# Performance work log

Measured on AMD Instinct MI355X. Metric: run time of the kernel, lower is better.

Reference implementation:

```python
import jax, jax.numpy as jnp
import numpy as np

B, IN_DIM, H1, H2, HID, SPEC_H, OUT, E = 16384, 1024, 2048, 2048, 1024, 2048, 1, 8


def setup_inputs() -> dict:
    key = jax.random.key(0)
    ks = jax.random.split(key, 12)

    def lin(k, fan_in, shape):
        # torch nn.Linear default init: U(-1/sqrt(fan_in), 1/sqrt(fan_in))
        bound = 1.0 / np.sqrt(fan_in)
        return jax.random.uniform(k, shape, jnp.float32, -bound, bound)

    return {
        "x": jax.random.normal(ks[0], (B, IN_DIM), jnp.float32),
        "d": jax.random.randint(ks[1], (B,), 0, E, jnp.int64),
        # shared encoder: Linear(IN,H1)+ReLU, Linear(H1,H2)+ReLU, Linear(H2,HID)
        "enc_W0": lin(ks[2], IN_DIM, (IN_DIM, H1)),
        "enc_b0": lin(ks[3], IN_DIM, (H1,)),
        "enc_W1": lin(ks[4], H1, (H1, H2)),
        "enc_b1": lin(ks[5], H1, (H2,)),
        "enc_W2": lin(ks[6], H2, (H2, HID)),
        "enc_b2": lin(ks[7], H2, (HID,)),
        # per-domain heads: Linear(HID,SPEC_H)+ReLU, Linear(SPEC_H,OUT)
        "spec_W1": lin(ks[8], HID, (E, HID, SPEC_H)),
        "spec_b1": lin(ks[9], HID, (E, SPEC_H)),
        "spec_W2": lin(ks[10], SPEC_H, (E, SPEC_H, OUT)),
        "spec_b2": lin(ks[11], SPEC_H, (E, OUT)),
    }


def reference(x, d, enc_W0, enc_b0, enc_W1, enc_b1, enc_W2, enc_b2,
              spec_W1, spec_b1, spec_W2, spec_b2):
    # Shared encoder (dropout is identity in eval mode)
    z = jax.nn.relu(x @ enc_W0 + enc_b0)        # [B, H1]
    z = jax.nn.relu(z @ enc_W1 + enc_b1)        # [B, H2]
    z = z @ enc_W2 + enc_b2                     # [B, HID]

    # Domain-routed heads: compute each expert on the full batch, combine by mask.
    n_experts = spec_W1.shape[0]
    out = jnp.zeros((z.shape[0], spec_W2.shape[-1]), dtype=z.dtype)  # [B, OUT]
    for e in range(n_experts):
        h = jax.nn.relu(z @ spec_W1[e] + spec_b1[e])  # [B, SPEC_H]
        y = h @ spec_W2[e] + spec_b2[e]               # [B, OUT]
        out = out + jnp.where((d == e)[:, None], y, jnp.zeros_like(y))
    return out
```

## Files before the change

### kernel.cpp

```cpp
#include <hip/hip_runtime.h>
#include <hip/hip_bf16.h>
#include <stdint.h>

#define B_SZ   16384
#define IN_DIM 1024
#define H1     2048
#define H2     2048
#define HID    1024
#define SPEC_H 2048
#define NE     8
#define ETILES 72

typedef __bf16 bf16x8 __attribute__((ext_vector_type(8)));
typedef float  f32x4  __attribute__((ext_vector_type(4)));
typedef ushort us8    __attribute__((ext_vector_type(8)));

__device__ __forceinline__ ushort f2bf(float f) {
  uint32_t u = __float_as_uint(f);
  u += 0x7FFF + ((u >> 16) & 1);
  return (ushort)(u >> 16);
}

__device__ __forceinline__ void gl_lds16(const void* g, void* l) {
  __builtin_amdgcn_global_load_lds(
      (const __attribute__((address_space(1))) void*)g,
      (__attribute__((address_space(3))) void*)l, 16, 0, 0);
}


struct TransDesc { const float* src; ushort* dst; int K, N, nx, base; };

struct PrepArgs {
  TransDesc td[4];
  const float* x; ushort* xb;
  const int* d; int* counts; const float* sb2; float* out;
  int castBase;
  int cntBase;
};

__global__ void prep_all(PrepArgs pa) {
  int g = blockIdx.x;
  int t = threadIdx.x;
  if (g >= pa.cntBase) {
    __shared__ int hist[NE];
    if (t < NE) hist[t] = 0;
    __syncthreads();
    int i = (g - pa.cntBase) * 256 + t;
    int e = pa.d[i];
    atomicAdd(&hist[e], 1);
    pa.out[i] = pa.sb2[e];
    __syncthreads();
    if (t < NE) atomicAdd(&pa.counts[t], hist[t]);
    return;
  }
  if (g >= pa.castBase) {
    size_t i = (size_t)(g - pa.castBase) * 4096 + (size_t)t * 16;
    float4 v0 = *(const float4*)(pa.x + i);
    float4 v1 = *(const float4*)(pa.x + i + 4);
    float4 v2 = *(const float4*)(pa.x + i + 8);
    float4 v3 = *(const float4*)(pa.x + i + 12);
    uint32_t p0 = f2bf(v0.x) | ((uint32_t)f2bf(v0.y) << 16);
    uint32_t p1 = f2bf(v0.z) | ((uint32_t)f2bf(v0.w) << 16);
    uint32_t p2 = f2bf(v1.x) | ((uint32_t)f2bf(v1.y) << 16);
    uint32_t p3 = f2bf(v1.z) | ((uint32_t)f2bf(v1.w) << 16);
    uint32_t p4 = f2bf(v2.x) | ((uint32_t)f2bf(v2.y) << 16);
    uint32_t p5 = f2bf(v2.z) | ((uint32_t)f2bf(v2.w) << 16);
    uint32_t p6 = f2bf(v3.x) | ((uint32_t)f2bf(v3.y) << 16);
    uint32_t p7 = f2bf(v3.z) | ((uint32_t)f2bf(v3.w) << 16);
    int4 pkA = {(int)p0, (int)p1, (int)p2, (int)p3};
    int4 pkB = {(int)p4, (int)p5, (int)p6, (int)p7};
    *(int4*)(pa.xb + i) = pkA;
    *(int4*)(pa.xb + i + 8) = pkB;
    return;
  }
  __shared__ float tile[64][65];
  int wsel = 0;
#pragma unroll
  for (int i = 1; i < 4; ++i)
    if (g >= pa.td[i].base) wsel = i;
  TransDesc dd = pa.td[wsel];
  int local = g - dd.base;
  int per = dd.nx * (dd.K >> 6);
  int z = local / per;
  int r = local - z * per;
  int bx = r % dd.nx, by = r / dd.nx;
  int n0 = bx * 64, k0 = by * 64;
  const float* src = dd.src + (size_t)z * dd.K * dd.N;
  ushort* dst = dd.dst + (size_t)z * dd.K * dd.N;
  int lk = t >> 4;
  int ln4 = (t & 15) * 4;
#pragma unroll
  for (int j = 0; j < 4; ++j) {
    int k = lk + j * 16;
    float4 v = *(const float4*)(src + (size_t)(k0 + k) * dd.N + n0 + ln4);
    tile[ln4 + 0][k] = v.x;
    tile[ln4 + 1][k] = v.y;
    tile[ln4 + 2][k] = v.z;
    tile[ln4 + 3][k] = v.w;
  }
  __syncthreads();
  int kc = (t & 7) * 8;
  int nb = t >> 3;
#pragma unroll
  for (int j = 0; j < 2; ++j) {
    int nn = nb + j * 32;
    us8 o;
#pragma unroll
    for (int q = 0; q < 8; ++q) o[q] = f2bf(tile[nn][kc + q]);
    *(us8*)(dst + (size_t)(n0 + nn) * dd.K + k0 + kc) = o;
  }
}


__global__ void build_k(const int* __restrict__ counts, int* __restrict__ catalog,
                        int* __restrict__ poff, int* __restrict__ cursors) {
  if (threadIdx.x == 0) {
    int off = 0;
    for (int e = 0; e < NE; ++e) {
      poff[e] = off * 256;
      int nt = (counts[e] + 255) >> 8;
      for (int i = 0; i < nt; ++i) catalog[off + i] = e;
      off += nt;
      cursors[e] = 0;
    }
    for (int i = off; i < ETILES; ++i) catalog[i] = -1;
  }
}

__global__ void scatter_k(const int* __restrict__ d, const int* __restrict__ poff,
                          int* __restrict__ cursors, int* __restrict__ perm) {
  __shared__ int wcnt[4][NE];
  __shared__ int basee[NE];
  int t = threadIdx.x;
  int i = blockIdx.x * 256 + t;
  int e = d[i];
  int w = t >> 6, lane = t & 63;
  uint64_t mymask = 0;
#pragma unroll
  for (int ee = 0; ee < NE; ++ee) {
    uint64_t mm = __ballot(e == ee);
    if (lane == 0) wcnt[w][ee] = __popcll(mm);
    if (e == ee) mymask = mm;
  }
  int rank = __popcll(mymask & ((1ull << lane) - 1ull));
  __syncthreads();
  if (t < NE) {
    int s = 0;
#pragma unroll
    for (int ww = 0; ww < 4; ++ww) { int c = wcnt[ww][t]; wcnt[ww][t] = s; s += c; }
    basee[t] = atomicAdd(&cursors[t], s);
  }
  __syncthreads();
  int pos = basee[e] + wcnt[w][e] + rank;
  perm[poff[e] + pos] = i;
}


template <int RELU>
__global__ __launch_bounds__(256, 2) void gemm_bias_256(
    const ushort* __restrict__ A, const ushort* __restrict__ Bt,
    const float* __restrict__ bias, ushort* __restrict__ C,
    int M, int N, int K, int lognx) {
  __shared__ __align__(16) ushort lA[256 * 64];
  __shared__ __align__(16) ushort lB[128 * 64];
  const int t = threadIdx.x;
  const int h = blockIdx.x;
  const int g = h >> 3;
  const int nx = 1 << lognx;
  const int by = (h & 7) + ((g >> lognx) << 3);
  const int bx = g & (nx - 1);
  const int m0 = by * 256, n0 = bx * 128;
  const int w = t >> 6, lane = t & 63;
  const int wm = (w >> 1) * 128, wn = (w & 1) * 64;
  const int q = lane >> 4, rl = lane & 15;

  f32x4 acc[8][4];
#pragma unroll
  for (int mi = 0; mi < 8; ++mi)
#pragma unroll
    for (int ni = 0; ni < 4; ++ni) acc[mi][ni] = 0.0f;

  const int row_s = t >> 3;
  const int pch_s = t & 7;

  for (int k0 = 0; k0 < K; k0 += 64) {
    __syncthreads();
#pragma unroll
    for (int j = 0; j < 8; ++j) {
      int row = j * 32 + row_s;
      int gch = pch_s ^ (row & 7);
      gl_lds16(A + (size_t)(m0 + row) * K + k0 + gch * 8, lA + j * 2048 + w * 512);
    }
#pragma unroll
    for (int j = 0; j < 4; ++j) {
      int row = j * 32 + row_s;
      int gch = pch_s ^ (row & 7);
      gl_lds16(Bt + (size_t)(n0 + row) * K + k0 + gch * 8, lB + j * 2048 + w * 512);
    }
    __syncthreads();
#pragma unroll
    for (int kk = 0; kk < 2; ++kk) {
      bf16x8 bfr[4];
#pragma unroll
      for (int i = 0; i < 4; ++i) {
        int pc = (kk * 4 + q) ^ (rl & 7);
        bfr[i] = __builtin_bit_cast(bf16x8, *(const int4*)(lB + (wn + i * 16 + rl) * 64 + pc * 8));
      }
#pragma unroll
      for (int mi = 0; mi < 8; ++mi) {
        int pc = (kk * 4 + q) ^ (rl & 7);
        bf16x8 af = __builtin_bit_cast(bf16x8, *(const int4*)(lA + (wm + mi * 16 + rl) * 64 + pc * 8));
#pragma unroll
        for (int ni = 0; ni < 4; ++ni)
          acc[mi][ni] = __builtin_amdgcn_mfma_f32_16x16x32_bf16(af, bfr[ni], acc[mi][ni], 0, 0, 0);
      }
    }
  }

  float bv[4];
#pragma unroll
  for (int ni = 0; ni < 4; ++ni) bv[ni] = bias[n0 + wn + ni * 16 + rl];
#pragma unroll
  for (int mi = 0; mi < 8; ++mi) {
    int rg = m0 + wm + mi * 16 + q * 4;
#pragma unroll
    for (int r = 0; r < 4; ++r) {
#pragma unroll
      for (int ni = 0; ni < 4; ++ni) {
        float v = acc[mi][ni][r] + bv[ni];
        if (RELU) v = fmaxf(v, 0.0f);
        C[(size_t)(rg + r) * N + n0 + wn + ni * 16 + rl] = f2bf(v);
      }
    }
  }
}


__global__ __launch_bounds__(256, 2) void expert_fused(
    const ushort* __restrict__ Z, const ushort* __restrict__ W1t,
    const float* __restrict__ b1, const float* __restrict__ w2,
    const int* __restrict__ perm, const int* __restrict__ catalog,
    const int* __restrict__ poff, const int* __restrict__ counts,
    float* __restrict__ out) {
  const int id = blockIdx.x;
  const int tile = (id & 7) * 9 + ((id >> 3) >> 4);
  const int ycol = (id >> 3) & 15;
  int e = catalog[tile];
  if (e < 0) return;
  __shared__ __align__(16) ushort lA[256 * 64];
  __shared__ __align__(16) ushort lB[128 * 64];
  __shared__ int perml[256];
  __shared__ float ysum[256];
  const int t = threadIdx.x;
  {
    int slot = tile * 256 + t;
    int rel = slot - poff[e];
    perml[t] = (rel < counts[e]) ? perm[slot] : -1;
    ysum[t] = 0.0f;
  }
  __syncthreads();

  const int n0 = ycol * 128;
  const ushort* Bt = W1t + (size_t)e * SPEC_H * HID;
  const float* b1e = b1 + (size_t)e * SPEC_H;
  const float* w2e = w2 + (size_t)e * SPEC_H;
  const int w = t >> 6, lane = t & 63;
  const int wm = (w >> 1) * 128, wn = (w & 1) * 64;
  const int q = lane >> 4, rl = lane & 15;

  f32x4 acc[8][4];
#pragma unroll
  for (int mi = 0; mi < 8; ++mi)
#pragma unroll
    for (int ni = 0; ni < 4; ++ni) acc[mi][ni] = 0.0f;

  const int row_s = t >> 3;
  const int pch_s = t & 7;

  for (int k0 = 0; k0 < HID; k0 += 64) {
    __syncthreads();
#pragma unroll
    for (int j = 0; j < 8; ++j) {
      int row = j * 32 + row_s;
      int gch = pch_s ^ (row & 7);
      int zr = perml[row];
      zr = zr < 0 ? 0 : zr;
      gl_lds16(Z + (size_t)zr * HID + k0 + gch * 8, lA + j * 2048 + w * 512);
    }
#pragma unroll
    for (int j = 0; j < 4; ++j) {
      int row = j * 32 + row_s;
      int gch = pch_s ^ (row & 7);
      gl_lds16(Bt + (size_t)(n0 + row) * HID + k0 + gch * 8, lB + j * 2048 + w * 512);
    }
    __syncthreads();
#pragma unroll
    for (int kk = 0; kk < 2; ++kk) {
      bf16x8 bfr[4];
#pragma unroll
      for (int i = 0; i < 4; ++i) {
        int pc = (kk * 4 + q) ^ (rl & 7);
        bfr[i] = __builtin_bit_cast(bf16x8, *(const int4*)(lB + (wn + i * 16 + rl) * 64 + pc * 8));
      }
#pragma unroll
      for (int mi = 0; mi < 8; ++mi) {
        int pc = (kk * 4 + q) ^ (rl & 7);
        bf16x8 af = __builtin_bit_cast(bf16x8, *(const int4*)(lA + (wm + mi * 16 + rl) * 64 + pc * 8));
#pragma unroll
        for (int ni = 0; ni < 4; ++ni)
          acc[mi][ni] = __builtin_amdgcn_mfma_f32_16x16x32_bf16(af, bfr[ni], acc[mi][ni], 0, 0, 0);
      }
    }
  }

  float w2v[4], b1v[4];
#pragma unroll
  for (int ni = 0; ni < 4; ++ni) {
    int n = n0 + wn + ni * 16 + rl;
    w2v[ni] = w2e[n];
    b1v[ni] = b1e[n];
  }
#pragma unroll
  for (int mi = 0; mi < 8; ++mi) {
#pragma unroll
    for (int r = 0; r < 4; ++r) {
      float p = 0.0f;
#pragma unroll
      for (int ni = 0; ni < 4; ++ni) {
        float h = acc[mi][ni][r] + b1v[ni];
        h = fmaxf(h, 0.0f);
        p += h * w2v[ni];
      }
      p += __shfl_xor(p, 1);
      p += __shfl_xor(p, 2);
      p += __shfl_xor(p, 4);
      p += __shfl_xor(p, 8);
      if (rl == 0) atomicAdd(&ysum[wm + mi * 16 + q * 4 + r], p);
    }
  }
  __syncthreads();
  {
    int orow = perml[t];
    if (orow >= 0) atomicAdd(&out[orow], ysum[t]);
  }
}


extern "C" void kernel_launch(void* const* d_in, const int* in_sizes, int n_in,
                              void* d_out, int out_size, void* d_ws, size_t ws_size,
                              hipStream_t stream) {
  const float* x   = (const float*)d_in[0];
  const int*   d   = (const int*)d_in[1];
  const float* eW0 = (const float*)d_in[2];
  const float* eb0 = (const float*)d_in[3];
  const float* eW1 = (const float*)d_in[4];
  const float* eb1 = (const float*)d_in[5];
  const float* eW2 = (const float*)d_in[6];
  const float* eb2 = (const float*)d_in[7];
  const float* sW1 = (const float*)d_in[8];
  const float* sb1 = (const float*)d_in[9];
  const float* sW2 = (const float*)d_in[10];
  const float* sb2 = (const float*)d_in[11];
  float* out = (float*)d_out;

  const size_t fixed = ((size_t)(4 + 8 + 4 + 32 + 32 + 32) << 20) + (1 << 20);
  int CH = 8192;
  if (ws_size >= fixed + (size_t)16384 * 8192) CH = 16384;

  char* p = (char*)d_ws;
  ushort* W0t  = (ushort*)p; p += (size_t)IN_DIM * H1 * 2;
  ushort* W1t  = (ushort*)p; p += (size_t)H1 * H2 * 2;
  ushort* W2t  = (ushort*)p; p += (size_t)H2 * HID * 2;
  ushort* sW1t = (ushort*)p; p += (size_t)NE * HID * SPEC_H * 2;
  ushort* Zb   = (ushort*)p; p += (size_t)B_SZ * HID * 2;
  ushort* xb   = (ushort*)p; p += (size_t)B_SZ * IN_DIM * 2;
  int* counts  = (int*)p; p += 64;
  int* cursors = (int*)p; p += 64;
  int* poff    = (int*)p; p += 64;
  int* catalog = (int*)p; p += 1024;
  int* perm    = (int*)p; p += (size_t)ETILES * 256 * 4;
  p = (char*)(((uintptr_t)p + 255) & ~(uintptr_t)255);
  ushort* z1 = (ushort*)p; p += (size_t)CH * H1 * 2;
  ushort* z2 = (ushort*)p; p += (size_t)CH * H2 * 2;

  hipMemsetAsync(counts, 0, 64, stream);

  PrepArgs pa;
  pa.td[0] = {eW0, W0t, IN_DIM, H1, H1 / 64, 0};
  pa.td[1] = {eW1, W1t, H1, H2, H2 / 64, 512};
  pa.td[2] = {eW2, W2t, H2, HID, HID / 64, 1536};
  pa.td[3] = {sW1, sW1t, HID, SPEC_H, SPEC_H / 64, 2048};
  pa.x = x; pa.xb = xb;
  pa.d = d; pa.counts = counts; pa.sb2 = sb2; pa.out = out;
  pa.castBase = 6144;
  pa.cntBase = 6144 + 4096;
  prep_all<<<6144 + 4096 + 64, 256, 0, stream>>>(pa);

  build_k<<<1, 64, 0, stream>>>(counts, catalog, poff, cursors);
  scatter_k<<<B_SZ / 256, 256, 0, stream>>>(d, poff, cursors, perm);

  for (int c = 0; c < B_SZ; c += CH) {
    gemm_bias_256<1><<<(CH / 256) * (H1 / 128), 256, 0, stream>>>(
        xb + (size_t)c * IN_DIM, W0t, eb0, z1, CH, H1, IN_DIM, 4);
    const int HM = CH / 2;
    gemm_bias_256<1><<<(HM / 256) * (H2 / 128), 256, 0, stream>>>(
        z1, W1t, eb1, z2, HM, H2, H1, 4);
    gemm_bias_256<1><<<(HM / 256) * (H2 / 128), 256, 0, stream>>>(
        z1 + (size_t)HM * H1, W1t, eb1, z2 + (size_t)HM * H2, HM, H2, H1, 4);
    gemm_bias_256<0><<<(CH / 256) * (HID / 128), 256, 0, stream>>>(
        z2, W2t, eb2, Zb + (size_t)c * HID, CH, HID, H2, 3);
  }

  expert_fused<<<ETILES * 16, 256, 0, stream>>>(
      Zb, sW1t, sb1, sW2, perm, catalog, poff, counts, out);
}
```

Before: 564.6 us.

## Scatter encoder output into expert-sorted layout and drop catalog build kernel

The last encoder GEMM now writes its rows straight to expert-sorted positions through an inverse permutation, so the expert kernel reads contiguous rows instead of gathering by perm. The single-thread build kernel is removed; tile offsets and expert assignment are recomputed from counts inside scatter_k and expert_fused. This saves one kernel launch and turns gathered reads into contiguous ones, at the cost of scattered row writes in the GEMM epilogue and a larger padded Z buffer.

```diff
diff --git a/kernel.cpp b/kernel.cpp
--- a/kernel.cpp
+++ b/kernel.cpp
@@ -112,29 +112,17 @@
 }
 
 
-__global__ void build_k(const int* __restrict__ counts, int* __restrict__ catalog,
-                        int* __restrict__ poff, int* __restrict__ cursors) {
-  if (threadIdx.x == 0) {
-    int off = 0;
-    for (int e = 0; e < NE; ++e) {
-      poff[e] = off * 256;
-      int nt = (counts[e] + 255) >> 8;
-      for (int i = 0; i < nt; ++i) catalog[off + i] = e;
-      off += nt;
-      cursors[e] = 0;
-    }
-    for (int i = off; i < ETILES; ++i) catalog[i] = -1;
-  }
-}
-
-__global__ void scatter_k(const int* __restrict__ d, const int* __restrict__ poff,
-                          int* __restrict__ cursors, int* __restrict__ perm) {
+__global__ void scatter_k(const int* __restrict__ d, const int* __restrict__ counts,
+                          int* __restrict__ cursors, int* __restrict__ perm,
+                          int* __restrict__ invperm) {
   __shared__ int wcnt[4][NE];
   __shared__ int basee[NE];
+  __shared__ int cnt_s[NE];
   int t = threadIdx.x;
   int i = blockIdx.x * 256 + t;
   int e = d[i];
   int w = t >> 6, lane = t & 63;
+  if (t < NE) cnt_s[t] = counts[t];
   uint64_t mymask = 0;
 #pragma unroll
   for (int ee = 0; ee < NE; ++ee) {
@@ -151,16 +139,24 @@
     basee[t] = atomicAdd(&cursors[t], s);
   }
   __syncthreads();
-  int pos = basee[e] + wcnt[w][e] + rank;
-  perm[poff[e] + pos] = i;
-}
-
-
-template <int RELU>
+  int acc8 = 0, poffe = 0;
+#pragma unroll
+  for (int ee = 0; ee < NE; ++ee) {
+    if (ee == e) poffe = acc8;
+    acc8 += (cnt_s[ee] + 255) >> 8;
+  }
+  poffe <<= 8;
+  int slot = poffe + basee[e] + wcnt[w][e] + rank;
+  perm[slot] = i;
+  invperm[i] = slot;
+}
+
+
+template <int RELU, int REMAP>
 __global__ __launch_bounds__(256, 2) void gemm_bias_256(
     const ushort* __restrict__ A, const ushort* __restrict__ Bt,
     const float* __restrict__ bias, ushort* __restrict__ C,
-    int M, int N, int K, int lognx) {
+    int M, int N, int K, int lognx, const int* __restrict__ rowmap) {
   __shared__ __align__(16) ushort lA[256 * 64];
   __shared__ __align__(16) ushort lB[128 * 64];
   const int t = threadIdx.x;
@@ -203,7 +199,7 @@
       bf16x8 bfr[4];
 #pragma unroll
       for (int i = 0; i < 4; ++i) {
-        int pc = (kk * 4 + q) ^ (rl & 7);
+        int pc = (kk * 4 + q) ^ (rl & 15 & 7);
         bfr[i] = __builtin_bit_cast(bf16x8, *(const int4*)(lB + (wn + i * 16 + rl) * 64 + pc * 8));
       }
 #pragma unroll
@@ -220,16 +216,37 @@
   float bv[4];
 #pragma unroll
   for (int ni = 0; ni < 4; ++ni) bv[ni] = bias[n0 + wn + ni * 16 + rl];
-#pragma unroll
-  for (int mi = 0; mi < 8; ++mi) {
-    int rg = m0 + wm + mi * 16 + q * 4;
-#pragma unroll
-    for (int r = 0; r < 4; ++r) {
-#pragma unroll
-      for (int ni = 0; ni < 4; ++ni) {
-        float v = acc[mi][ni][r] + bv[ni];
-        if (RELU) v = fmaxf(v, 0.0f);
-        C[(size_t)(rg + r) * N + n0 + wn + ni * 16 + rl] = f2bf(v);
+
+  if constexpr (REMAP) {
+    __shared__ int rml[256];
+    rml[t] = rowmap[m0 + t];
+    __syncthreads();
+#pragma unroll
+    for (int mi = 0; mi < 8; ++mi) {
+      int rg_l = wm + mi * 16 + q * 4;
+#pragma unroll
+      for (int r = 0; r < 4; ++r) {
+        int drow = rml[rg_l + r];
+#pragma unroll
+        for (int ni = 0; ni < 4; ++ni) {
+          float v = acc[mi][ni][r] + bv[ni];
+          if (RELU) v = fmaxf(v, 0.0f);
+          C[(size_t)drow * N + n0 + wn + ni * 16 + rl] = f2bf(v);
+        }
+      }
+    }
+  } else {
+#pragma unroll
+    for (int mi = 0; mi < 8; ++mi) {
+      int rg = m0 + wm + mi * 16 + q * 4;
+#pragma unroll
+      for (int r = 0; r < 4; ++r) {
+#pragma unroll
+        for (int ni = 0; ni < 4; ++ni) {
+          float v = acc[mi][ni][r] + bv[ni];
+          if (RELU) v = fmaxf(v, 0.0f);
+          C[(size_t)(rg + r) * N + n0 + wn + ni * 16 + rl] = f2bf(v);
+        }
       }
     }
   }
@@ -237,15 +254,21 @@
 
 
 __global__ __launch_bounds__(256, 2) void expert_fused(
-    const ushort* __restrict__ Z, const ushort* __restrict__ W1t,
+    const ushort* __restrict__ Zp, const ushort* __restrict__ W1t,
     const float* __restrict__ b1, const float* __restrict__ w2,
-    const int* __restrict__ perm, const int* __restrict__ catalog,
-    const int* __restrict__ poff, const int* __restrict__ counts,
+    const int* __restrict__ perm, const int* __restrict__ counts,
     float* __restrict__ out) {
   const int id = blockIdx.x;
   const int tile = (id & 7) * 9 + ((id >> 3) >> 4);
   const int ycol = (id >> 3) & 15;
-  int e = catalog[tile];
+  int tbase = 0, e = -1, poffe = 0, cnte = 0;
+#pragma unroll
+  for (int ee = 0; ee < NE; ++ee) {
+    int c = counts[ee];
+    int nt = (c + 255) >> 8;
+    if (tile >= tbase && tile < tbase + nt) { e = ee; poffe = tbase << 8; cnte = c; }
+    tbase += nt;
+  }
   if (e < 0) return;
   __shared__ __align__(16) ushort lA[256 * 64];
   __shared__ __align__(16) ushort lB[128 * 64];
@@ -254,12 +277,12 @@
   const int t = threadIdx.x;
   {
     int slot = tile * 256 + t;
-    int rel = slot - poff[e];
-    perml[t] = (rel < counts[e]) ? perm[slot] : -1;
+    int rel = slot - poffe;
+    perml[t] = (rel < cnte) ? perm[slot] : -1;
     ysum[t] = 0.0f;
   }
-  __syncthreads();
-
+
+  const int m0 = tile * 256;
   const int n0 = ycol * 128;
   const ushort* Bt = W1t + (size_t)e * SPEC_H * HID;
   const float* b1e = b1 + (size_t)e * SPEC_H;
@@ -283,9 +306,7 @@
     for (int j = 0; j < 8; ++j) {
       int row = j * 32 + row_s;
       int gch = pch_s ^ (row & 7);
-      int zr = perml[row];
-      zr = zr < 0 ? 0 : zr;
-      gl_lds16(Z + (size_t)zr * HID + k0 + gch * 8, lA + j * 2048 + w * 512);
+      gl_lds16(Zp + (size_t)(m0 + row) * HID + k0 + gch * 8, lA + j * 2048 + w * 512);
     }
 #pragma unroll
     for (int j = 0; j < 4; ++j) {
@@ -363,7 +384,7 @@
   const float* sb2 = (const float*)d_in[11];
   float* out = (float*)d_out;
 
-  const size_t fixed = ((size_t)(4 + 8 + 4 + 32 + 32 + 32) << 20) + (1 << 20);
+  const size_t fixed = ((size_t)(4 + 8 + 4 + 32 + 36 + 32) << 20) + (1 << 20);
   int CH = 8192;
   if (ws_size >= fixed + (size_t)16384 * 8192) CH = 16384;
 
@@ -372,18 +393,17 @@
   ushort* W1t  = (ushort*)p; p += (size_t)H1 * H2 * 2;
   ushort* W2t  = (ushort*)p; p += (size_t)H2 * HID * 2;
   ushort* sW1t = (ushort*)p; p += (size_t)NE * HID * SPEC_H * 2;
-  ushort* Zb   = (ushort*)p; p += (size_t)B_SZ * HID * 2;
+  ushort* Zp   = (ushort*)p; p += (size_t)ETILES * 256 * HID * 2;
   ushort* xb   = (ushort*)p; p += (size_t)B_SZ * IN_DIM * 2;
   int* counts  = (int*)p; p += 64;
   int* cursors = (int*)p; p += 64;
-  int* poff    = (int*)p; p += 64;
-  int* catalog = (int*)p; p += 1024;
   int* perm    = (int*)p; p += (size_t)ETILES * 256 * 4;
+  int* invperm = (int*)p; p += (size_t)B_SZ * 4;
   p = (char*)(((uintptr_t)p + 255) & ~(uintptr_t)255);
   ushort* z1 = (ushort*)p; p += (size_t)CH * H1 * 2;
   ushort* z2 = (ushort*)p; p += (size_t)CH * H2 * 2;
 
-  hipMemsetAsync(counts, 0, 64, stream);
+  hipMemsetAsync(counts, 0, 128, stream);
 
   PrepArgs pa;
   pa.td[0] = {eW0, W0t, IN_DIM, H1, H1 / 64, 0};
@@ -396,21 +416,20 @@
   pa.cntBase = 6144 + 4096;
   prep_all<<<6144 + 4096 + 64, 256, 0, stream>>>(pa);
 
-  build_k<<<1, 64, 0, stream>>>(counts, catalog, poff, cursors);
-  scatter_k<<<B_SZ / 256, 256, 0, stream>>>(d, poff, cursors, perm);
+  scatter_k<<<B_SZ / 256, 256, 0, stream>>>(d, counts, cursors, perm, invperm);
 
   for (int c = 0; c < B_SZ; c += CH) {
-    gemm_bias_256<1><<<(CH / 256) * (H1 / 128), 256, 0, stream>>>(
-        xb + (size_t)c * IN_DIM, W0t, eb0, z1, CH, H1, IN_DIM, 4);
+    gemm_bias_256<1, 0><<<(CH / 256) * (H1 / 128), 256, 0, stream>>>(
+        xb + (size_t)c * IN_DIM, W0t, eb0, z1, CH, H1, IN_DIM, 4, nullptr);
     const int HM = CH / 2;
-    gemm_bias_256<1><<<(HM / 256) * (H2 / 128), 256, 0, stream>>>(
-        z1, W1t, eb1, z2, HM, H2, H1, 4);
-    gemm_bias_256<1><<<(HM / 256) * (H2 / 128), 256, 0, stream>>>(
-        z1 + (size_t)HM * H1, W1t, eb1, z2 + (size_t)HM * H2, HM, H2, H1, 4);
-    gemm_bias_256<0><<<(CH / 256) * (HID / 128), 256, 0, stream>>>(
-        z2, W2t, eb2, Zb + (size_t)c * HID, CH, HID, H2, 3);
+    gemm_bias_256<1, 0><<<(HM / 256) * (H2 / 128), 256, 0, stream>>>(
+        z1, W1t, eb1, z2, HM, H2, H1, 4, nullptr);
+    gemm_bias_256<1, 0><<<(HM / 256) * (H2 / 128), 256, 0, stream>>>(
+        z1 + (size_t)HM * H1, W1t, eb1, z2 + (size_t)HM * H2, HM, H2, H1, 4, nullptr);
+    gemm_bias_256<0, 1><<<(CH / 256) * (HID / 128), 256, 0, stream>>>(
+        z2, W2t, eb2, Zp, CH, HID, H2, 3, invperm + c);
   }
 
   expert_fused<<<ETILES * 16, 256, 0, stream>>>(
-      Zb, sW1t, sb1, sW2, perm, catalog, poff, counts, out);
-}
+      Zp, sW1t, sb1, sW2, perm, counts, out);
+}
```

New measurement: 566.1 us. No clear change (+0.3%).
